# Kernel tuning notes

Hardware: AMD Instinct MI355X
Metric: run time of the kernel (lower is better)

The kernel has to match this reference:

```python
import jax, jax.numpy as jnp
from jax import lax
import numpy as np

N, M, S = 16, 32, 128
ALPHA = 1e-06


def _conv(x, w, b, stride):
    y = lax.conv_general_dilated(x, w, (stride, stride), [(1, 1), (1, 1)],
                                 dimension_numbers=('NCHW', 'OIHW', 'NCHW'))
    return y + b[None, :, None, None]


def _deconv(x, w, b):
    # torch ConvTranspose2d(k=4, s=2, p=1); torch weight layout [in, out, kh, kw]
    k = jnp.transpose(w, (1, 0, 2, 3))[:, :, ::-1, ::-1]
    y = lax.conv_general_dilated(x, k, (1, 1), [(2, 2), (2, 2)],
                                 lhs_dilation=(2, 2),
                                 dimension_numbers=('NCHW', 'OIHW', 'NCHW'))
    return y + b[None, :, None, None]


def _kaiming(key, shape):
    fan_in = shape[1] * shape[2] * shape[3]
    return jax.random.normal(key, shape, dtype=jnp.float32) * np.float32(np.sqrt(2.0 / fan_in))


def setup_inputs():
    key = jax.random.key(0)
    ks = jax.random.split(key, 12)
    B, H, W = 8, 256, 256
    return {
        'x': jax.random.normal(ks[0], (B, 3, H, W), dtype=jnp.float32),
        'e0n_w1': _kaiming(ks[1], (N, 3, 3, 3)), 'e0n_b1': jnp.zeros((N,), jnp.float32),
        'e0n_w2': _kaiming(ks[2], (N, N, 3, 3)), 'e0n_b2': jnp.zeros((N,), jnp.float32),
        'e0s_w1': _kaiming(ks[3], (S, 3, 3, 3)), 'e0s_b1': jnp.zeros((S,), jnp.float32),
        'e0s_w2': _kaiming(ks[4], (S, S, 3, 3)), 'e0s_b2': jnp.zeros((S,), jnp.float32),
        'd0_dw': jax.random.normal(ks[5], (S, 3, 4, 4), jnp.float32) * np.float32(np.sqrt(2.0 / (3 * 16))),
        'd0_db': jnp.zeros((3,), jnp.float32),
        'd0_cw': _kaiming(ks[6], (3, 3, 3, 3)), 'd0_cb': jnp.zeros((3,), jnp.float32),
        'cell_k': jax.random.normal(ks[7], (M, N), jnp.float32) / np.float32(np.sqrt(N)),
        'cell_v': jax.random.normal(ks[8], (M, S), jnp.float32) / np.float32(np.sqrt(S)),
    }


def reference(x, e0n_w1, e0n_b1, e0n_w2, e0n_b2, e0s_w1, e0s_b1, e0s_w2, e0s_b2,
              d0_dw, d0_db, d0_cw, d0_cb, cell_k, cell_v):
    silu = jax.nn.silu
    # ConvBlock encoders (stride-2 on second conv)
    e0_n = silu(_conv(silu(_conv(x, e0n_w1, e0n_b1, 1)), e0n_w2, e0n_b2, 2))  # [B,N,H/2,W/2]
    e0_s = silu(_conv(silu(_conv(x, e0s_w1, e0s_b1, 1)), e0s_w2, e0s_b2, 2))  # [B,S,H/2,W/2]
    B, _, H, W = e0_n.shape
    # permute+flatten to token streams (the irregular-access glue)
    z = e0_n.transpose(0, 2, 3, 1).reshape(-1, N)        # [T, N]
    t_star = e0_s.transpose(0, 2, 3, 1).reshape(-1, S)   # [T, S]
    # memcell: softmax key/value retrieval over M slots
    w = jax.nn.softmax(z @ cell_k.T / jnp.sqrt(jnp.float32(N)), axis=-1)  # [T, M]
    t_hat = w @ cell_v                                   # read_update's read (old memory)
    cell_v_new = cell_v + ALPHA * (w.T @ (t_star - t_hat))  # delta-rule value update
    t_read = w @ cell_v_new                              # read(); d1_n == e0_n so weights reused
    d0_m = t_read.reshape(B, H, W, S).transpose(0, 3, 1, 2)  # [B,S,H/2,W/2]
    # DeconvBlock decoder back to 3 channels at full resolution
    d0_n = silu(_conv(silu(_deconv(d0_m, d0_dw, d0_db)), d0_cw, d0_cb, 1))
    return d0_n
```

## Files before the change

kernel.cpp:

```cpp
#include <hip/hip_runtime.h>
#include <hip/hip_bf16.h>


#define ALPHA_F 1e-6f
#define TTOT 131072

typedef __attribute__((ext_vector_type(8))) short bf16x8;
typedef __attribute__((ext_vector_type(4))) float f32x4;

__device__ __forceinline__ float silu_f(float x) {
    return x * __builtin_amdgcn_rcpf(1.f + __expf(-x));
}

__device__ __forceinline__ short f2bf(float f) {
    __hip_bfloat16 h = __float2bfloat16(f);
    union { __hip_bfloat16 b; short s; } u; u.b = h; return u.s;
}

__device__ __forceinline__ float bf2f(unsigned short s) {
    union { unsigned u; float f; } c; c.u = (unsigned)s << 16; return c.f;
}

__device__ __forceinline__ int pack_fp8x4(float a, float b, float c, float d) {
    int lo = __builtin_amdgcn_cvt_pk_fp8_f32(a, b, 0, false);
    return  __builtin_amdgcn_cvt_pk_fp8_f32(c, d, lo, true);
}

template<int CO>
__global__ __launch_bounds__(256) void conv1_silu(
    const float* __restrict__ x, const float* __restrict__ wgt,
    const float* __restrict__ bias, float* __restrict__ out)
{
    int idx = blockIdx.x * 256 + threadIdx.x;
    int w = idx & 255, h = (idx >> 8) & 255, b = idx >> 16;
    const float* xb = x + (size_t)b * 3 * 65536;
    float in[27];
#pragma unroll
    for (int ci = 0; ci < 3; ci++)
#pragma unroll
        for (int ky = 0; ky < 3; ky++)
#pragma unroll
            for (int kx = 0; kx < 3; kx++) {
                int hh = h + ky - 1, ww = w + kx - 1;
                bool ok = ((unsigned)hh < 256u) && ((unsigned)ww < 256u);
                in[(ci * 3 + ky) * 3 + kx] = ok ? xb[(ci << 16) + (hh << 8) + ww] : 0.f;
            }
    float* ob = out + (size_t)b * CO * 65536 + (h << 8) + w;
#pragma unroll 4
    for (int co = 0; co < CO; co++) {
        float acc = bias[co];
#pragma unroll
        for (int k = 0; k < 27; k++) acc += in[k] * wgt[co * 27 + k];
        ob[(size_t)co << 16] = silu_f(acc);
    }
}

__global__ __launch_bounds__(256) void conv1n_silu(
    const float* __restrict__ x, const float* __restrict__ wgt,
    const float* __restrict__ bias, float* __restrict__ anc)
{
    int idx = blockIdx.x * 256 + threadIdx.x;
    int w = idx & 255, h = (idx >> 8) & 255, b = idx >> 16;
    const float* xb = x + (size_t)b * 3 * 65536;
    float in[27];
#pragma unroll
    for (int ci = 0; ci < 3; ci++)
#pragma unroll
        for (int ky = 0; ky < 3; ky++)
#pragma unroll
            for (int kx = 0; kx < 3; kx++) {
                int hh = h + ky - 1, ww = w + kx - 1;
                bool ok = ((unsigned)hh < 256u) && ((unsigned)ww < 256u);
                in[(ci * 3 + ky) * 3 + kx] = ok ? xb[(ci << 16) + (hh << 8) + ww] : 0.f;
            }
    float o[16];
#pragma unroll
    for (int co = 0; co < 16; co++) {
        float acc = bias[co];
#pragma unroll
        for (int k = 0; k < 27; k++) acc += in[k] * wgt[co * 27 + k];
        o[co] = silu_f(acc);
    }
    float* ob = anc + (((size_t)b * 258 + (h + 1)) * 264 + (w + 1)) * 16;
#pragma unroll
    for (int j = 0; j < 4; j++) *(float4*)&ob[4 * j] = *(float4*)&o[4 * j];
}

#define XPAD_DW 842112
__global__ __launch_bounds__(256) void sprep_kern(
    const float* __restrict__ x, const float* __restrict__ w1,
    const float* __restrict__ w2n,
    unsigned* __restrict__ xpad, unsigned* __restrict__ wbf,
    float* __restrict__ wn, float* __restrict__ anc)
{
    if (blockIdx.x >= 3291) {
        int zidx = (blockIdx.x - 3291) * 256 + threadIdx.x;
        int b = zidx / 8352, j = zidx % 8352;
        size_t off;
        if (j < 4224) {
            int c = j >> 4, ci = j & 15;
            off = (((size_t)b * 258 + 0) * 264 + c) * 16 + ci;
        } else {
            int j2 = j - 4224;
            int r = j2 >> 4, ci = j2 & 15;
            off = (((size_t)b * 258 + r) * 264 + 0) * 16 + ci;
        }
        anc[off] = 0.f;
        return;
    }
    if (blockIdx.x == 3290) {
        int t = threadIdx.x;
        if (t < 128) {
            int co = t;
            unsigned short row[28];
#pragma unroll
            for (int k = 0; k < 27; k++) row[k] = (unsigned short)f2bf(w1[co * 27 + k]);
            row[27] = 0;
#pragma unroll
            for (int j = 0; j < 14; j++)
                wbf[co * 20 + j] = (unsigned)row[2 * j] | ((unsigned)row[2 * j + 1] << 16);
#pragma unroll
            for (int j = 14; j < 20; j++) wbf[co * 20 + j] = 0u;
        }
#pragma unroll
        for (int u = 0; u < 9; u++) {
            int i = t * 9 + u;
            int co = i & 15, ci = (i >> 4) & 15, k = i >> 8;
            wn[i] = w2n[(co * 16 + ci) * 9 + k];
        }
        return;
    }
    int d = blockIdx.x * 256 + threadIdx.x;
    if (d >= XPAD_DW) return;
    int w2 = d % 136;
    int rr = d / 136;
    int hp = rr % 258;
    int plane = rr / 258;
    unsigned val = 0u;
    if (hp >= 1 && hp <= 256 && w2 >= 4 && w2 <= 131) {
        const float* src = x + (size_t)plane * 65536 + (size_t)(hp - 1) * 256 + (2 * w2 - 8);
        float2 f = *(const float2*)src;
        val = (unsigned)(unsigned short)f2bf(f.x) |
              ((unsigned)(unsigned short)f2bf(f.y) << 16);
    }
    xpad[d] = val;
}

#define C1K 40
__global__ __launch_bounds__(256) void conv1s_mfma(
    const unsigned short* __restrict__ xpad, const unsigned short* __restrict__ wbf,
    const float* __restrict__ bias, char* __restrict__ out8)
{
    __shared__ __align__(16) short Ps[128 * C1K];
    int tid = threadIdx.x;
    int g = blockIdx.x;
    int b = g >> 10, rem = g & 1023;
    int hh2 = rem >> 1;
    int h = hh2 >> 1, w0 = (hh2 & 1) * 128;
    int coB = (rem & 1) * 64;

    int lane = tid & 63, wave = tid >> 6;
    int coL = (wave & 1) * 32, pxH = (wave >> 1) * 64;
    int r16 = lane & 15, q = lane >> 4, koff = q * 8;

    bf16x8 af[2];
#pragma unroll
    for (int mt = 0; mt < 2; mt++)
        af[mt] = *(const bf16x8*)&wbf[(coB + coL + mt * 16 + r16) * C1K + koff];

    if (tid < 128) {
        int wpix = w0 + tid;
        const unsigned short* p0 = xpad + ((size_t)(b * 3) * 258 + h) * 272 + 7 + wpix;
        unsigned v[27];
#pragma unroll
        for (int ci = 0; ci < 3; ci++) {
            const unsigned short* pc = p0 + ci * 70176;
#pragma unroll
            for (int ky = 0; ky < 3; ky++)
#pragma unroll
                for (int kx = 0; kx < 3; kx++)
                    v[ci * 9 + ky * 3 + kx] = pc[ky * 272 + kx];
        }
        unsigned dw[16];
#pragma unroll
        for (int i = 0; i < 13; i++) dw[i] = v[2 * i] | (v[2 * i + 1] << 16);
        dw[13] = v[26];
        dw[14] = 0u; dw[15] = 0u;
#pragma unroll
        for (int j = 0; j < 4; j++)
            *(float4*)&Ps[tid * C1K + j * 8] = *(float4*)&dw[j * 4];
    }
    __syncthreads();

    bf16x8 bfr[4];
#pragma unroll
    for (int nt = 0; nt < 4; nt++)
        bfr[nt] = *(bf16x8*)&Ps[(pxH + nt * 16 + r16) * C1K + koff];
    f32x4 acc[2][4];
#pragma unroll
    for (int mt = 0; mt < 2; mt++)
#pragma unroll
        for (int nt = 0; nt < 4; nt++) {
#pragma unroll
            for (int r = 0; r < 4; r++) acc[mt][nt][r] = 0.f;
            acc[mt][nt] = __builtin_amdgcn_mfma_f32_16x16x32_bf16(
                af[mt], bfr[nt], acc[mt][nt], 0, 0, 0);
        }

    int hwb = (h << 8) + w0 + pxH;
    int* ob4 = (int*)out8 + (size_t)b * 8 * 65536 * 4;
#pragma unroll
    for (int mt = 0; mt < 2; mt++) {
        int cb = coB + coL + mt * 16 + q * 4;
        float4 bv = *(const float4*)&bias[cb];
        int cg = (coB + coL + mt * 16) >> 4;
#pragma unroll
        for (int nt = 0; nt < 4; nt++) {
            int hw = hwb + nt * 16 + r16;
            int pk = pack_fp8x4(silu_f(acc[mt][nt][0] + bv.x),
                                silu_f(acc[mt][nt][1] + bv.y),
                                silu_f(acc[mt][nt][2] + bv.z),
                                silu_f(acc[mt][nt][3] + bv.w));
            ob4[((size_t)cg * 65536 + hw) * 4 + q] = pk;
        }
    }
}

__global__ __launch_bounds__(256) void wprep_kern(
    const float* __restrict__ w, int* __restrict__ wt8)
{
    int d = blockIdx.x * 256 + threadIdx.x;
    int pos = d >> 12;
    int rb = (d << 2) & 16383;
    int c16 = rb >> 11, co = (rb >> 4) & 127, e0 = rb & 15;
    float f[4];
#pragma unroll
    for (int j = 0; j < 4; j++) {
        int ci = c16 * 16 + e0 + j;
        f[j] = w[co * 1152 + ci * 9 + pos];
    }
    wt8[d] = pack_fp8x4(f[0], f[1], f[2], f[3]);
}

__global__ __launch_bounds__(256) void conv2s_mfma(
    const char* __restrict__ a8,
    const char* __restrict__ wt8,
    const float* __restrict__ bias, __hip_bfloat16* __restrict__ out)
{
    __shared__ __align__(16) char As[2][4096];
    __shared__ __align__(16) char Bs[2][8192];
    int tid = threadIdx.x;
    int g = (blockIdx.x & 7) * 256 + (blockIdx.x >> 3);
    int b = g >> 8, h2 = (g >> 1) & 127, w2base = (g & 1) * 64;
    int lane = tid & 63, wave = tid >> 6;
    int mrow = lane & 15, q = lane >> 4;

    f32x4 acc[2][4];
#pragma unroll
    for (int i = 0; i < 2; i++)
#pragma unroll
        for (int j = 0; j < 4; j++)
#pragma unroll
            for (int r = 0; r < 4; r++) acc[i][j][r] = 0.f;

    const float4* ab4 = (const float4*)a8 + (size_t)b * 8 * 65536;
    const float4* wb4 = (const float4*)wt8;
    int cA = tid >> 6, tokA = tid & 63;
    int sB0 = tid, sB1 = tid + 256;
    int swT = tid & 8;
    int offA = ((q & 1) * 8) ^ (mrow & 8);

    int ps = (h2 == 0) ? 3 : 0;
    int nst = (9 - ps) * 2;

#define C2S_LOAD(s, ra, rb0, rb1) do {                                      \
        int pos_ = ps + ((s) >> 1), cc_ = (s) & 1;                          \
        int ky_ = pos_ / 3, kx_ = pos_ - 3 * ky_;                           \
        int y_ = 2 * h2 - 1 + ky_;                                          \
        int x_ = 2 * (w2base + tokA) - 1 + kx_;                             \
        int pix_ = (y_ << 8) + (x_ & 255);                                  \
        ra = make_float4(0.f, 0.f, 0.f, 0.f);                               \
        if (x_ >= 0) ra = ab4[(size_t)(cc_ * 4 + cA) * 65536 + pix_];       \
        const float4* brow_ = wb4 + pos_ * 1024 + cc_ * 512;                \
        rb0 = brow_[sB0]; rb1 = brow_[sB1];                                 \
    } while (0)

#define C2S_STORE(bufi, ra, rb0, rb1) do {                                  \
        union { float4 v; long l[2]; } uA_, u0_, u1_;                       \
        uA_.v = ra; u0_.v = rb0; u1_.v = rb1;                               \
        *(long*)&As[bufi][tid * 16 + swT]       = uA_.l[0];                 \
        *(long*)&As[bufi][tid * 16 + (8 ^ swT)] = uA_.l[1];                 \
        *(long*)&Bs[bufi][sB0 * 16 + swT]       = u0_.l[0];                 \
        *(long*)&Bs[bufi][sB0 * 16 + (8 ^ swT)] = u0_.l[1];                 \
        *(long*)&Bs[bufi][sB1 * 16 + swT]       = u1_.l[0];                 \
        *(long*)&Bs[bufi][sB1 * 16 + (8 ^ swT)] = u1_.l[1];                 \
    } while (0)

#define C2S_BAR() do {                                                      \
        asm volatile("s_waitcnt lgkmcnt(0)" ::: "memory");                  \
        __builtin_amdgcn_s_barrier();                                       \
        asm volatile("" ::: "memory");                                      \
    } while (0)

    auto compute = [&](const char* Ab, const char* Bb) {
#pragma unroll
        for (int kc = 0; kc < 2; kc++) {
            int cl = kc * 2 + (q >> 1);
            long afr[4], bfr[2];
#pragma unroll
            for (int mt = 0; mt < 4; mt++)
                afr[mt] = *(const long*)&Ab[(cl * 64 + mt * 16 + mrow) * 16 + offA];
#pragma unroll
            for (int nt = 0; nt < 2; nt++)
                bfr[nt] = *(const long*)&Bb[(cl * 128 + wave * 32 + nt * 16 + mrow) * 16 + offA];
#pragma unroll
            for (int nt = 0; nt < 2; nt++)
#pragma unroll
                for (int mt = 0; mt < 4; mt++)
                    acc[nt][mt] = __builtin_amdgcn_mfma_f32_16x16x32_fp8_fp8(
                        afr[mt], bfr[nt], acc[nt][mt], 0, 0, 0);
        }
    };

    float4 a0, b00, b01, a1, b10, b11;
    C2S_LOAD(0, a0, b00, b01);
    C2S_STORE(0, a0, b00, b01);
    C2S_LOAD(1, a1, b10, b11);
    C2S_BAR();

    for (int s = 0; s < nst; s += 2) {
        if (s + 2 < nst) C2S_LOAD(s + 2, a0, b00, b01);
        compute(As[0], Bs[0]);
        C2S_STORE(1, a1, b10, b11);
        C2S_BAR();
        if (s + 3 < nst) C2S_LOAD(s + 3, a1, b10, b11);
        compute(As[1], Bs[1]);
        if (s + 2 < nst) C2S_STORE(0, a0, b00, b01);
        C2S_BAR();
    }
#undef C2S_LOAD
#undef C2S_STORE
#undef C2S_BAR

    int rowg = q * 4;
    size_t tbase = (size_t)g * 64;
#pragma unroll
    for (int nt = 0; nt < 2; nt++) {
        int co = wave * 32 + nt * 16 + mrow;
        float bvs = bias[co];
#pragma unroll
        for (int mt = 0; mt < 4; mt++)
#pragma unroll
            for (int r = 0; r < 4; r++) {
                int m = mt * 16 + rowg + r;
                out[(tbase + m) * 128 + co] =
                    __float2bfloat16(silu_f(acc[nt][mt][r] + bvs));
            }
    }
}

__global__ __launch_bounds__(256) void conv2n_fused(
    const float* __restrict__ anc, const float* __restrict__ wn,
    const float* __restrict__ bias, const float* __restrict__ ck,
    float* __restrict__ wout)
{
    int idx = blockIdx.x * 256 + threadIdx.x;
    int w2 = idx & 127, h2 = (idx >> 7) & 127, b = idx >> 14;
    const float* pb = anc + (((size_t)b * 258 + 2 * h2) * 264 + 2 * w2) * 16;
    float4 tv[9][4];
#pragma unroll
    for (int ky = 0; ky < 3; ky++)
#pragma unroll
        for (int kx = 0; kx < 3; kx++) {
            const float* tp = pb + (ky * 264 + kx) * 16;
#pragma unroll
            for (int j = 0; j < 4; j++)
                tv[ky * 3 + kx][j] = *(const float4*)&tp[4 * j];
        }
    float acc[16];
#pragma unroll
    for (int co = 0; co < 16; co++) acc[co] = bias[co];
#pragma unroll
    for (int k = 0; k < 9; k++) {
        float tap[16];
#pragma unroll
        for (int j = 0; j < 4; j++) *(float4*)&tap[4 * j] = tv[k][j];
        const float* wk = wn + k * 256;
#pragma unroll
        for (int ci = 0; ci < 16; ci++) {
            float tvv = tap[ci];
#pragma unroll
            for (int co = 0; co < 16; co++)
                acc[co] += tvv * wk[ci * 16 + co];
        }
    }
    float zv[16];
#pragma unroll
    for (int co = 0; co < 16; co++) zv[co] = silu_f(acc[co]);
    float lg[32]; float mx = -1e30f;
#pragma unroll
    for (int m = 0; m < 32; m++) {
        float a = 0.f;
#pragma unroll
        for (int n = 0; n < 16; n++) a += zv[n] * ck[m * 16 + n];
        a *= 0.25f;
        lg[m] = a; mx = fmaxf(mx, a);
    }
    float s = 0.f;
#pragma unroll
    for (int m = 0; m < 32; m++) { lg[m] = __expf(lg[m] - mx); s += lg[m]; }
    float inv = 1.f / s;
    float4* wp = (float4*)(wout + (size_t)idx * 32);
#pragma unroll
    for (int m = 0; m < 8; m++)
        wp[m] = make_float4(lg[4 * m] * inv, lg[4 * m + 1] * inv,
                            lg[4 * m + 2] * inv, lg[4 * m + 3] * inv);
}

__global__ __launch_bounds__(256) void memcell_acc_kern(
    const float* __restrict__ wmat, const __hip_bfloat16* __restrict__ tstar,
    float* __restrict__ part)
{
    __shared__ float ws[64][32];
    __shared__ float ts[64 * 128];
    int tid = threadIdx.x;
    int sg = tid & 31, mg = tid >> 5;
    int mW = tid & 31, m2 = (tid >> 5) * 4;
    float accT[16], accW[4];
#pragma unroll
    for (int i = 0; i < 16; i++) accT[i] = 0.f;
#pragma unroll
    for (int i = 0; i < 4; i++) accW[i] = 0.f;

#pragma unroll 1
    for (int cc = 0; cc < 2; cc++) {
        int c = blockIdx.x * 2 + cc;
        size_t base = (size_t)c * 64;
        __syncthreads();
        {
            const float4* src = (const float4*)(wmat + base * 32);
            float4* dst = (float4*)&ws[0][0];
#pragma unroll
            for (int i = 0; i < 2; i++) dst[tid + 256 * i] = src[tid + 256 * i];
            const float4* src2 = (const float4*)(tstar + base * 128);
#pragma unroll
            for (int i = 0; i < 4; i++) {
                union { float4 v; unsigned short us[8]; } u;
                u.v = src2[tid + 256 * i];
                float* d = &ts[(tid + 256 * i) * 8];
                float4 lo = make_float4(bf2f(u.us[0]), bf2f(u.us[1]), bf2f(u.us[2]), bf2f(u.us[3]));
                float4 hi = make_float4(bf2f(u.us[4]), bf2f(u.us[5]), bf2f(u.us[6]), bf2f(u.us[7]));
                *(float4*)d = lo; *(float4*)(d + 4) = hi;
            }
        }
        __syncthreads();
        for (int t = 0; t < 64; t++) {
            float4 wv = *(const float4*)&ws[t][mg * 4];
            float4 sv = *(const float4*)&ts[t * 128 + sg * 4];
            accT[0]  += wv.x * sv.x; accT[1]  += wv.x * sv.y; accT[2]  += wv.x * sv.z; accT[3]  += wv.x * sv.w;
            accT[4]  += wv.y * sv.x; accT[5]  += wv.y * sv.y; accT[6]  += wv.y * sv.z; accT[7]  += wv.y * sv.w;
            accT[8]  += wv.z * sv.x; accT[9]  += wv.z * sv.y; accT[10] += wv.z * sv.z; accT[11] += wv.z * sv.w;
            accT[12] += wv.w * sv.x; accT[13] += wv.w * sv.y; accT[14] += wv.w * sv.z; accT[15] += wv.w * sv.w;
            float wa = ws[t][mW];
            float4 wb = *(const float4*)&ws[t][m2];
            accW[0] += wa * wb.x; accW[1] += wa * wb.y;
            accW[2] += wa * wb.z; accW[3] += wa * wb.w;
        }
    }
    float* pb = part + (size_t)blockIdx.x * 5120;
#pragma unroll
    for (int i = 0; i < 16; i++) pb[i * 256 + tid] = accT[i];
#pragma unroll
    for (int i = 0; i < 4; i++) pb[4096 + i * 256 + tid] = accW[i];
}

__global__ __launch_bounds__(256) void memcell_reduce_kern(
    const float* __restrict__ part, float* __restrict__ WtT, float* __restrict__ WtW)
{
    int gid = blockIdx.x * 256 + threadIdx.x;
    int j = gid % 5120, seg = gid / 5120;
    const float* p = part + (size_t)seg * 64 * 5120 + j;
    float s = 0.f;
#pragma unroll 8
    for (int k = 0; k < 64; k++) s += p[(size_t)k * 5120];
    int i = j >> 8, t = j & 255;
    if (j < 4096) {
        int sg = t & 31, mg = t >> 5;
        atomicAdd(&WtT[(mg * 4 + (i >> 2)) * 128 + sg * 4 + (i & 3)], s);
    } else {
        int i2 = i - 16;
        int mW = t & 31, m2 = (t >> 5) * 4;
        atomicAdd(&WtW[mW * 32 + m2 + i2], s);
    }
}

__global__ __launch_bounds__(256) void cvnew_kern(
    const float* __restrict__ cv, const float* __restrict__ WtW,
    const float* __restrict__ WtT, float* __restrict__ cvn)
{
    int idx = blockIdx.x * 256 + threadIdx.x;
    int s = idx & 127, m = idx >> 7;
    float g = WtT[idx];
#pragma unroll
    for (int j = 0; j < 32; j++) g -= WtW[m * 32 + j] * cv[j * 128 + s];
    cvn[idx] = cv[idx] + ALPHA_F * g;
}

__global__ __launch_bounds__(256) void emat_kern(
    const float* __restrict__ cvn, const float* __restrict__ dw, float* __restrict__ E)
{
    int idx = blockIdx.x * 256 + threadIdx.x;
    int m = idx >> 6, j = idx & 63;
    int pos = j >> 2, co = j & 3;
    float s = 0.f;
    if (co < 3) {
        const float* cv = cvn + m * 128;
        for (int ci = 0; ci < 128; ci++)
            s += cv[ci] * dw[ci * 48 + co * 16 + pos];
    }
    E[idx] = s;
}

__global__ __launch_bounds__(256) void tread64_kern(
    const float* __restrict__ wmat, const float* __restrict__ E, float* __restrict__ t64)
{
    int t = blockIdx.x * 256 + threadIdx.x;
    float wv[32];
    const float4* wp = (const float4*)(wmat + (size_t)t * 32);
#pragma unroll
    for (int i = 0; i < 8; i++) {
        float4 v = wp[i];
        wv[4 * i] = v.x; wv[4 * i + 1] = v.y; wv[4 * i + 2] = v.z; wv[4 * i + 3] = v.w;
    }
    f32x4 acc[16];
#pragma unroll
    for (int i = 0; i < 16; i++)
#pragma unroll
        for (int r = 0; r < 4; r++) acc[i][r] = 0.f;
    const f32x4* E4 = (const f32x4*)E;
#pragma unroll 4
    for (int m = 0; m < 32; m++) {
        float wm = wv[m];
#pragma unroll
        for (int i = 0; i < 16; i++) {
            f32x4 e = E4[m * 16 + i];
#pragma unroll
            for (int r = 0; r < 4; r++) acc[i][r] += wm * e[r];
        }
    }
    f32x4* ob = (f32x4*)t64;
#pragma unroll
    for (int i = 0; i < 16; i++)
        ob[(size_t)i * TTOT + t] = acc[i];
}

__global__ __launch_bounds__(256) void dec_gather_kern(
    const float* __restrict__ t64, const float* __restrict__ db, float* __restrict__ out)
{
    int g = blockIdx.x;
    int wb = g & 7, hb = (g >> 3) & 7, b = g >> 6;
    int tx = threadIdx.x & 15, ty = threadIdx.x >> 4;
    int h2 = hb * 16 + ty, w2 = wb * 16 + tx;

    float mh[3], mw[3];
    int ihc[3], iwc[3];
#pragma unroll
    for (int a = 0; a < 3; a++) {
        int v = h2 - 1 + a;
        mh[a] = ((unsigned)v < 128u) ? 1.f : 0.f;
        ihc[a] = v < 0 ? 0 : (v > 127 ? 127 : v);
        v = w2 - 1 + a;
        mw[a] = ((unsigned)v < 128u) ? 1.f : 0.f;
        iwc[a] = v < 0 ? 0 : (v > 127 ? 127 : v);
    }
    float acc[2][2][3];
#pragma unroll
    for (int ph = 0; ph < 2; ph++)
#pragma unroll
        for (int pw = 0; pw < 2; pw++)
#pragma unroll
            for (int co = 0; co < 3; co++) acc[ph][pw][co] = db[co];

    const int RA[4] = {0, 1, 1, 2}, RP[4] = {0, 0, 1, 1}, RK[4] = {3, 1, 2, 0};
    size_t tokb = (size_t)b * 16384;
#pragma unroll
    for (int ri = 0; ri < 4; ri++)
#pragma unroll
        for (int cj = 0; cj < 4; cj++) {
            int a = RA[ri], c = RA[cj];
            float m = mh[a] * mw[c];
            size_t tok = tokb + (ihc[a] << 7) + iwc[c];
            int pos = RK[ri] * 4 + RK[cj];
            float4 v = *(const float4*)&t64[((size_t)pos * TTOT + tok) * 4];
            int ph = RP[ri], pw = RP[cj];
            acc[ph][pw][0] += m * v.x;
            acc[ph][pw][1] += m * v.y;
            acc[ph][pw][2] += m * v.z;
        }
    int h = 2 * h2, w = 2 * w2;
#pragma unroll
    for (int ph = 0; ph < 2; ph++)
#pragma unroll
        for (int co = 0; co < 3; co++) {
            float2 v = make_float2(silu_f(acc[ph][0][co]), silu_f(acc[ph][1][co]));
            *(float2*)&out[(size_t)b * 3 * 65536 + (size_t)co * 65536 + ((size_t)(h + ph) << 8) + w] = v;
        }
}

extern "C" void kernel_launch(void* const* d_in, const int* in_sizes, int n_in,
                              void* d_out, int out_size, void* d_ws, size_t ws_size,
                              hipStream_t stream)
{
    const float* x      = (const float*)d_in[0];
    const float* e0n_w1 = (const float*)d_in[1];
    const float* e0n_b1 = (const float*)d_in[2];
    const float* e0n_w2 = (const float*)d_in[3];
    const float* e0n_b2 = (const float*)d_in[4];
    const float* e0s_w1 = (const float*)d_in[5];
    const float* e0s_b1 = (const float*)d_in[6];
    const float* e0s_w2 = (const float*)d_in[7];
    const float* e0s_b2 = (const float*)d_in[8];
    const float* d0_dw  = (const float*)d_in[9];
    const float* d0_db  = (const float*)d_in[10];
    const float* d0_cw  = (const float*)d_in[11];
    const float* d0_cb  = (const float*)d_in[12];
    const float* cell_k = (const float*)d_in[13];
    const float* cell_v = (const float*)d_in[14];
    float* outp = (float*)d_out;

    char* ws = (char*)d_ws;
    char* a_s8             = ws;
    __hip_bfloat16* t_star = (__hip_bfloat16*)(ws + 134217728);
    char* wt8     = (char*)(ws + 201326592);
    float* part   = (float*)(ws + 201850880);
    float* Emat   = (float*)(ws + 224000000);
    float* wmat   = (float*)(ws + 243269632);
    float* WtW    = (float*)(ws + 260046848);
    float* WtT    = (float*)(ws + 260050944);
    float* cvn    = (float*)(ws + 260067328);
    float* t64    = (float*)(ws);
    float* dec1   = (float*)(ws + 67108864);
    unsigned* xpad = (unsigned*)(ws + 73400320);
    unsigned* wbf  = (unsigned*)(ws + 76800000);
    float* wn      = (float*)(ws + 76810240);
    float* a_nc    = (float*)(ws + 77594624);

    sprep_kern<<<3552, 256, 0, stream>>>(x, e0s_w1, e0n_w2, xpad, wbf, wn, a_nc);
    conv1n_silu<<<2048, 256, 0, stream>>>(x, e0n_w1, e0n_b1, a_nc);
    conv2n_fused<<<512, 256, 0, stream>>>(a_nc, wn, e0n_b2, cell_k, wmat);
    wprep_kern<<<144, 256, 0, stream>>>(e0s_w2, (int*)wt8);
    conv1s_mfma<<<8192, 256, 0, stream>>>((const unsigned short*)xpad,
                                          (const unsigned short*)wbf, e0s_b1, a_s8);
    conv2s_mfma<<<2048, 256, 0, stream>>>(a_s8, wt8, e0s_b2, t_star);
    hipMemsetAsync(WtW, 0, (1024 + 4096) * sizeof(float), stream);
    memcell_acc_kern<<<1024, 256, 0, stream>>>(wmat, t_star, part);
    memcell_reduce_kern<<<320, 256, 0, stream>>>(part, WtT, WtW);
    cvnew_kern<<<16, 256, 0, stream>>>(cell_v, WtW, WtT, cvn);
    emat_kern<<<8, 256, 0, stream>>>(cvn, d0_dw, Emat);
    tread64_kern<<<512, 256, 0, stream>>>(wmat, Emat, t64);
    dec_gather_kern<<<512, 256, 0, stream>>>(t64, d0_db, dec1);
    conv1_silu<3><<<2048, 256, 0, stream>>>(dec1, d0_cw, d0_cb, outp);
}
```

Baseline: 281.5 us.

## Fuse memory read projection into deconv gather to drop t64 intermediate

Replaces the tread64 kernel, which computed a 64-wide projection per token and wrote a large intermediate buffer, with an on-the-fly computation inside the deconv gather kernel. Each thread loads the 9 neighbouring token weight rows, double-buffered, and computes only the positions it needs against E. This removes a large global-memory write and its later read. In exchange, each token's weights are reread by several neighbouring threads, and each thread does more ALU work and uses more registers.

New measurement: 347.5 us. 23.4% more time.

```diff
diff --git a/kernel.cpp b/kernel.cpp
--- a/kernel.cpp
+++ b/kernel.cpp
@@ -521,41 +521,9 @@
     E[idx] = s;
 }
 
-__global__ __launch_bounds__(256) void tread64_kern(
-    const float* __restrict__ wmat, const float* __restrict__ E, float* __restrict__ t64)
-{
-    int t = blockIdx.x * 256 + threadIdx.x;
-    float wv[32];
-    const float4* wp = (const float4*)(wmat + (size_t)t * 32);
-#pragma unroll
-    for (int i = 0; i < 8; i++) {
-        float4 v = wp[i];
-        wv[4 * i] = v.x; wv[4 * i + 1] = v.y; wv[4 * i + 2] = v.z; wv[4 * i + 3] = v.w;
-    }
-    f32x4 acc[16];
-#pragma unroll
-    for (int i = 0; i < 16; i++)
-#pragma unroll
-        for (int r = 0; r < 4; r++) acc[i][r] = 0.f;
-    const f32x4* E4 = (const f32x4*)E;
-#pragma unroll 4
-    for (int m = 0; m < 32; m++) {
-        float wm = wv[m];
-#pragma unroll
-        for (int i = 0; i < 16; i++) {
-            f32x4 e = E4[m * 16 + i];
-#pragma unroll
-            for (int r = 0; r < 4; r++) acc[i][r] += wm * e[r];
-        }
-    }
-    f32x4* ob = (f32x4*)t64;
-#pragma unroll
-    for (int i = 0; i < 16; i++)
-        ob[(size_t)i * TTOT + t] = acc[i];
-}
-
-__global__ __launch_bounds__(256) void dec_gather_kern(
-    const float* __restrict__ t64, const float* __restrict__ db, float* __restrict__ out)
+__global__ __launch_bounds__(256) void dec_fused_kern(
+    const float* __restrict__ wmat, const float* __restrict__ E,
+    const float* __restrict__ db, float* __restrict__ out)
 {
     int g = blockIdx.x;
     int wb = g & 7, hb = (g >> 3) & 7, b = g >> 6;
@@ -581,22 +549,62 @@
 #pragma unroll
             for (int co = 0; co < 3; co++) acc[ph][pw][co] = db[co];
 
-    const int RA[4] = {0, 1, 1, 2}, RP[4] = {0, 0, 1, 1}, RK[4] = {3, 1, 2, 0};
+    const f32x4* E4 = (const f32x4*)E;
     size_t tokb = (size_t)b * 16384;
-#pragma unroll
-    for (int ri = 0; ri < 4; ri++)
-#pragma unroll
-        for (int cj = 0; cj < 4; cj++) {
-            int a = RA[ri], c = RA[cj];
-            float m = mh[a] * mw[c];
-            size_t tok = tokb + (ihc[a] << 7) + iwc[c];
-            int pos = RK[ri] * 4 + RK[cj];
-            float4 v = *(const float4*)&t64[((size_t)pos * TTOT + tok) * 4];
-            int ph = RP[ri], pw = RP[cj];
-            acc[ph][pw][0] += m * v.x;
-            acc[ph][pw][1] += m * v.y;
-            acc[ph][pw][2] += m * v.z;
-        }
+
+    const int RL[3][2] = {{0, 0}, {1, 2}, {3, 3}};
+    const int RN[3] = {1, 2, 1};
+    const int RP[4] = {0, 0, 1, 1}, RK[4] = {3, 1, 2, 0};
+
+    float4 bufA[8], bufB[8];
+#define DEC_LOADROW(k, buf) do {                                            \
+        int ia_ = (k) / 3, ic_ = (k) % 3;                                   \
+        size_t tok_ = tokb + ((size_t)ihc[ia_] << 7) + iwc[ic_];            \
+        const float4* wp_ = (const float4*)(wmat + tok_ * 32);              \
+        _Pragma("unroll")                                                   \
+        for (int j = 0; j < 8; j++) (buf)[j] = wp_[j];                      \
+    } while (0)
+
+    DEC_LOADROW(0, bufA);
+#pragma unroll
+    for (int k = 0; k < 9; k++) {
+        float4* cur = (k & 1) ? bufB : bufA;
+        float4* nxt = (k & 1) ? bufA : bufB;
+        if (k < 8) DEC_LOADROW(k + 1, nxt);
+        float wv[32];
+#pragma unroll
+        for (int j = 0; j < 8; j++) {
+            wv[4 * j] = cur[j].x; wv[4 * j + 1] = cur[j].y;
+            wv[4 * j + 2] = cur[j].z; wv[4 * j + 3] = cur[j].w;
+        }
+        int ia = k / 3, ic = k % 3;
+        float mk = mh[ia] * mw[ic];
+#pragma unroll
+        for (int u = 0; u < 2; u++) {
+            if (u >= RN[ia]) break;
+#pragma unroll
+            for (int vv = 0; vv < 2; vv++) {
+                if (vv >= RN[ic]) break;
+                int ri = RL[ia][u], cj = RL[ic][vv];
+                int pos = RK[ri] * 4 + RK[cj];
+                f32x4 v;
+#pragma unroll
+                for (int r = 0; r < 4; r++) v[r] = 0.f;
+#pragma unroll
+                for (int m = 0; m < 32; m++) {
+                    f32x4 e = E4[m * 16 + pos];
+#pragma unroll
+                    for (int r = 0; r < 4; r++) v[r] += wv[m] * e[r];
+                }
+                int ph = RP[ri], pw = RP[cj];
+                acc[ph][pw][0] += mk * v[0];
+                acc[ph][pw][1] += mk * v[1];
+                acc[ph][pw][2] += mk * v[2];
+            }
+        }
+    }
+#undef DEC_LOADROW
+
     int h = 2 * h2, w = 2 * w2;
 #pragma unroll
     for (int ph = 0; ph < 2; ph++)
@@ -638,7 +646,6 @@
     float* WtW    = (float*)(ws + 260046848);
     float* WtT    = (float*)(ws + 260050944);
     float* cvn    = (float*)(ws + 260067328);
-    float* t64    = (float*)(ws);
     float* dec1   = (float*)(ws + 67108864);
     unsigned* xpad = (unsigned*)(ws + 73400320);
     unsigned* wbf  = (unsigned*)(ws + 76800000);
@@ -657,7 +664,6 @@
     memcell_reduce_kern<<<320, 256, 0, stream>>>(part, WtT, WtW);
     cvnew_kern<<<16, 256, 0, stream>>>(cell_v, WtW, WtT, cvn);
     emat_kern<<<8, 256, 0, stream>>>(cvn, d0_dw, Emat);
-    tread64_kern<<<512, 256, 0, stream>>>(wmat, Emat, t64);
-    dec_gather_kern<<<512, 256, 0, stream>>>(t64, d0_db, dec1);
+    dec_fused_kern<<<512, 256, 0, stream>>>(wmat, Emat, d0_db, dec1);
     conv1_silu<3><<<2048, 256, 0, stream>>>(dec1, d0_cw, d0_cb, outp);
 }
```
